# Optimization experiments

Measured on AMD Instinct MI355X. Metric: run time of the kernel, lower is better.

Reference implementation:

```python
import jax, jax.numpy as jnp
import numpy as np

B, N, E = 2, 16384, 262144          # batch, nodes, directed edges (avg deg 16)
K, D, Wm = 256, 3, 1                # nmodes, ndims, nmeasures
C, L, FC = 128, 4, 128              # channels, Fourier layers, fc hidden
IN_DIM, OUT_DIM = 3, 1


def setup_inputs() -> dict:
    key = jax.random.key(0)
    ks = jax.random.split(key, 20)
    s = 1.0 / (C * C)
    inp = {
        "x": jax.random.normal(ks[0], (B, N, IN_DIM), jnp.float32),
        "nodes": jax.random.uniform(ks[1], (B, N, D), jnp.float32),
        "node_mask": jnp.ones((B, N, 1), jnp.float32),
        "node_weights": jax.random.uniform(ks[2], (B, N, Wm), jnp.float32) / N,
        "directed_edges": jax.random.randint(ks[3], (B, E, 2), 0, N),
        "edge_gradient_weights": jax.random.normal(ks[4], (B, E, D), jnp.float32),
        "modes": jax.random.normal(ks[5], (K, D, Wm), jnp.float32),
        "sp_L": jnp.ones((D, Wm), jnp.float32),
        "weights_c": s * jax.random.uniform(ks[6], (L, C, C, K, Wm), jnp.float32),
        "weights_s": s * jax.random.uniform(ks[7], (L, C, C, K, Wm), jnp.float32),
        "weights_0": s * jax.random.uniform(ks[8], (L, C, C, 1, Wm), jnp.float32),
        "fc0_w": jax.random.normal(ks[9], (C, IN_DIM), jnp.float32) * 0.1,
        "fc0_b": jnp.zeros((C,), jnp.float32),
        "ws_w": jax.random.normal(ks[10], (L, C, C), jnp.float32) * 0.05,
        "ws_b": jnp.zeros((L, C), jnp.float32),
        "gws_w": jax.random.normal(ks[11], (L, C, D * C), jnp.float32) * 0.05,
        "gws_b": jnp.zeros((L, C), jnp.float32),
        "fc1_w": jax.random.normal(ks[12], (FC, C), jnp.float32) * 0.05,
        "fc1_b": jnp.zeros((FC,), jnp.float32),
        "fc2_w": jax.random.normal(ks[13], (OUT_DIM, FC), jnp.float32) * 0.05,
        "fc2_b": jnp.zeros((OUT_DIM,), jnp.float32),
    }
    return inp


def _gelu(x):
    return jax.nn.gelu(x, approximate=False)  # torch F.gelu default = exact erf


def _compute_gradient(f, directed_edges, edge_gradient_weights):
    # f: [B, C, N] -> gradients [B, C*D, N] via directed-edge scatter-add
    fT = jnp.transpose(f, (0, 2, 1))                       # [B, N, C]
    tgt, src = directed_edges[..., 0], directed_edges[..., 1]
    f_src = jnp.take_along_axis(fT, src[..., None], axis=1)  # [B, E, C]
    f_tgt = jnp.take_along_axis(fT, tgt[..., None], axis=1)
    msg = jnp.einsum('bed,bec->becd', edge_gradient_weights, f_src - f_tgt)
    msg = msg.reshape(msg.shape[0], msg.shape[1], -1)        # [B, E, C*D]

    def scat(m, t):
        return jnp.zeros((fT.shape[1], m.shape[-1]), m.dtype).at[t].add(m)

    g = jax.vmap(scat)(msg, tgt)                             # [B, N, C*D]
    return jnp.transpose(g, (0, 2, 1))


def _spectral_conv(x, wc, wsn, w0, bc, bs, b0, wbc, wbs, wb0):
    # x: [B, C_in, N]
    xc = jnp.einsum('bix,bxkw->bikw', x, wbc)
    xs = -jnp.einsum('bix,bxkw->bikw', x, wbs)
    x0 = jnp.einsum('bix,bxkw->bikw', x, wb0)
    fc = jnp.einsum('bikw,iokw->bokw', xc, wc) - jnp.einsum('bikw,iokw->bokw', xs, wsn)
    fs = jnp.einsum('bikw,iokw->bokw', xs, wc) + jnp.einsum('bikw,iokw->bokw', xc, wsn)
    f0 = jnp.einsum('bikw,iokw->bokw', x0, w0)
    return (jnp.einsum('bokw,bxkw->box', f0, b0)
            + 2.0 * jnp.einsum('bokw,bxkw->box', fc, bc)
            - 2.0 * jnp.einsum('bokw,bxkw->box', fs, bs))


def reference(x, nodes, node_mask, node_weights, directed_edges, edge_gradient_weights,
              modes, sp_L, weights_c, weights_s, weights_0,
              fc0_w, fc0_b, ws_w, ws_b, gws_w, gws_b, fc1_w, fc1_b, fc2_w, fc2_b):
    # Fourier bases with learnable length-scale sp_L: [K,D,Wm]*[D,Wm]
    temp = jnp.einsum('bxd,kdw->bxkw', nodes, modes * sp_L)   # [B,N,K,Wm]
    bc, bs = jnp.cos(temp), jnp.sin(temp)
    b0 = jnp.zeros((temp.shape[0], temp.shape[1], 1, temp.shape[3]), temp.dtype)
    nw = (node_weights * node_mask)[:, :, None, :]            # [B,N,1,Wm]
    wbc, wbs, wb0 = bc * nw, bs * nw, b0 * nw

    h = jnp.einsum('bxi,ci->bxc', x, fc0_w) + fc0_b           # lift [B,N,C]
    h = jnp.transpose(h, (0, 2, 1))                           # [B,C,N]

    for i in range(L):
        x1 = _spectral_conv(h, weights_c[i], weights_s[i], weights_0[i],
                            bc, bs, b0, wbc, wbs, wb0)
        x2 = jnp.einsum('oc,bcn->bon', ws_w[i], h) + ws_b[i][None, :, None]
        grad = _compute_gradient(h, directed_edges, edge_gradient_weights)
        x3 = jnp.einsum('og,bgn->bon', gws_w[i], grad) + gws_b[i][None, :, None]
        h = x1 + x2 + x3
        if i != L - 1:
            h = _gelu(h)

    h = jnp.transpose(h, (0, 2, 1))                           # [B,N,C]
    h = _gelu(jnp.einsum('bnc,fc->bnf', h, fc1_w) + fc1_b)
    out = jnp.einsum('bnf,of->bno', h, fc2_w) + fc2_b         # [B,N,out_dim]
    return out
```

## Files before the change

### kernel.cpp

```cpp
#include <hip/hip_runtime.h>
#include <math.h>

#define Bn 2
#define Nn 16384
#define En 262144
#define Kn 256
#define Cn 128
#define Rn 512
#define Ln 4
#define LDP 72
#define NSPLIT 64

typedef float f32x4 __attribute__((ext_vector_type(4)));
typedef short s16x8 __attribute__((ext_vector_type(8)));

__device__ __forceinline__ float gelu_f(float x){
  return 0.5f*x*(1.0f + erff(x*0.70710678118654752440f));
}
__device__ __forceinline__ unsigned short f2b(float x){
  unsigned int u = __float_as_uint(x);
  unsigned int r = (u + 0x7FFFu + ((u>>16)&1u)) >> 16;
  return (unsigned short)r;
}
__device__ __forceinline__ float b2f(unsigned short h){
  return __uint_as_float(((unsigned int)h)<<16);
}
__device__ __forceinline__ unsigned int pack2(float lo, float hi){
  return (unsigned int)f2b(lo) | ((unsigned int)f2b(hi) << 16);
}


__global__ __launch_bounds__(256) void k_nw(const float* __restrict__ nwt,
                                            const float* __restrict__ msk,
                                            float* __restrict__ nw){
  int i = blockIdx.x*256 + threadIdx.x;
  nw[i] = nwt[i]*msk[i];
}

__global__ __launch_bounds__(256) void k_basis(const float* __restrict__ nodes,
                                               const float* __restrict__ modes,
                                               const float* __restrict__ spl,
                                               unsigned short* __restrict__ basis,
                                               unsigned short* __restrict__ basisT){
  __shared__ unsigned short tile[32*520];
  int gn0 = blockIdx.x*32;
  int tid = threadIdx.x;
  float m0 = modes[tid*3+0]*spl[0];
  float m1 = modes[tid*3+1]*spl[1];
  float m2 = modes[tid*3+2]*spl[2];
  for (int j=0;j<32;j++){
    const float* nd = nodes + (size_t)(gn0+j)*3;
    float t = nd[0]*m0 + nd[1]*m1 + nd[2]*m2;
    float s,c;
    sincosf(t,&s,&c);
    tile[j*520 + tid]       = f2b(c);
    tile[j*520 + 256 + tid] = f2b(s);
  }
  __syncthreads();
  int row = tid>>3, col0 = (tid&7)*64;
  #pragma unroll
  for (int q=0;q<8;q++){
    s16x8 v = *(const s16x8*)&tile[row*520 + col0 + q*8];
    *(s16x8*)(basis + (size_t)(gn0+row)*Rn + col0 + q*8) = v;
  }
  int b = gn0 >> 14;
  int nl = gn0 & (Nn-1);
  #pragma unroll
  for (int h=0; h<2; h++){
    int r = h*256 + tid;
    unsigned short* dst = basisT + ((size_t)(b*Rn + r))*Nn + nl;
    #pragma unroll
    for (int q=0;q<4;q++){
      unsigned short tmp[8];
      #pragma unroll
      for (int e=0;e<8;e++) tmp[e] = tile[(q*8+e)*520 + r];
      *(s16x8*)(dst + q*8) = *(const s16x8*)tmp;
    }
  }
}

__global__ __launch_bounds__(256) void k_lift(const float* __restrict__ x,
                                              const float* __restrict__ w,
                                              const float* __restrict__ bias,
                                              const float* __restrict__ nw,
                                              unsigned short* __restrict__ hg,
                                              unsigned short* __restrict__ hpack,
                                              unsigned short* __restrict__ hwT){
  __shared__ float ht[64*132];
  int gn0 = blockIdx.x*64;
  int tid = threadIdx.x;
  int c = tid & 127, rh = tid >> 7;
  float w0 = w[c*3], w1 = w[c*3+1], w2 = w[c*3+2], bb = bias[c];
  for (int j=0;j<32;j++){
    int n = rh*32 + j;
    const float* xp = x + (size_t)(gn0+n)*3;
    float v = bb + xp[0]*w0 + xp[1]*w1 + xp[2]*w2;
    ht[n*132 + c] = v;
    unsigned short hv = f2b(v);
    hg[(size_t)(gn0+n)*Rn + c] = hv;
    hpack[(size_t)(gn0+n)*Cn + c] = hv;
  }
  __syncthreads();
  int b = gn0 >> 14, nl = gn0 & (Nn-1);
  int cc = tid>>1, hf = tid&1;
  unsigned short* dst = hwT + ((size_t)(b*Cn + cc))*Nn + nl + hf*32;
  #pragma unroll
  for (int q=0;q<8;q++){
    int n = hf*32 + q*4;
    float4 nv = *(const float4*)&nw[(size_t)b*Nn + nl + n];
    ushort4 pk;
    pk.x = f2b(ht[(n+0)*132+cc]*nv.x);
    pk.y = f2b(ht[(n+1)*132+cc]*nv.y);
    pk.z = f2b(ht[(n+2)*132+cc]*nv.z);
    pk.w = f2b(ht[(n+3)*132+cc]*nv.w);
    *(ushort4*)(dst + q*4) = pk;
  }
}

__global__ __launch_bounds__(128) void k_w2c(const float* __restrict__ ws_w,
                                             const float* __restrict__ ws_b,
                                             const float* __restrict__ gws_w,
                                             const float* __restrict__ gws_b,
                                             unsigned short* __restrict__ W2,
                                             float* __restrict__ bias2){
  int bid = blockIdx.x;
  int tid = threadIdx.x;
  unsigned short* wrow = W2 + (size_t)bid*Rn;
  wrow[tid] = f2b(ws_w[(size_t)bid*Cn + tid]);
  const float* g = gws_w + (size_t)bid*384;
  wrow[128+tid] = f2b(g[tid*3+0]);
  wrow[256+tid] = f2b(g[tid*3+1]);
  wrow[384+tid] = f2b(g[tid*3+2]);
  if (tid==0) bias2[bid] = ws_b[bid] + gws_b[bid];
}

__global__ __launch_bounds__(256) void k_cvt(const float* __restrict__ in,
                                             unsigned short* __restrict__ out, int n){
  int i = blockIdx.x*256 + threadIdx.x;
  if (i < n) out[i] = f2b(in[i]);
}


__global__ __launch_bounds__(256) void k_count(const int* __restrict__ de,
                                               int* __restrict__ cnt){
  int i = blockIdx.x*256 + threadIdx.x;
  int b = i >> 18;
  int tgt = de[(size_t)i*2];
  atomicAdd(&cnt[b*Nn + tgt], 1);
}

__global__ __launch_bounds__(1024) void k_scan(const int* __restrict__ cnt,
                                               int* __restrict__ rowptr,
                                               int* __restrict__ cursor){
  __shared__ int part[1024];
  int t = threadIdx.x;
  int b = t >> 9;
  int li = t & 511;
  int loc[32];
  int s = 0;
  int base = b*Nn + li*32;
  #pragma unroll
  for (int j=0;j<32;j++){ loc[j] = s; s += cnt[base+j]; }
  part[t] = s;
  __syncthreads();
  int run = s;
  for (int off=1; off<512; off<<=1){
    int v = (li >= off) ? part[t-off] : 0;
    __syncthreads();
    part[t] += v;
    __syncthreads();
  }
  int incl = part[t];
  int excl = incl - run;
  int rbase = b*(Nn+1) + li*32;
  #pragma unroll
  for (int j=0;j<32;j++){
    int val = excl + loc[j];
    rowptr[rbase+j] = val;
    cursor[base+j]  = val;
  }
  if (li == 511) rowptr[b*(Nn+1) + Nn] = incl;
}

__global__ __launch_bounds__(256) void k_fill(const int* __restrict__ de,
                                              const float* __restrict__ egw,
                                              int* __restrict__ cursor,
                                              float4* __restrict__ epack){
  int i = blockIdx.x*256 + threadIdx.x;
  int b = i >> 18;
  int tgt = de[(size_t)i*2];
  int src = de[(size_t)i*2+1];
  int pos = atomicAdd(&cursor[b*Nn + tgt], 1);
  const float* g = egw + (size_t)i*3;
  float4 pk;
  pk.x = __int_as_float(src);
  pk.y = g[0]; pk.z = g[1]; pk.w = g[2];
  epack[(size_t)b*En + pos] = pk;
}

__global__ __launch_bounds__(128) void k_grad(const unsigned short* __restrict__ hpack,
                                              const float4* __restrict__ epack,
                                              const int* __restrict__ rowptr,
                                              unsigned short* __restrict__ hg_w){
  int bid = blockIdx.x;
  int b = bid >> 14, n = bid & (Nn-1);
  int tid = threadIdx.x;
  int wv = tid >> 6;
  int l  = tid & 63;
  const unsigned short* hb = hpack + (size_t)b*Nn*Cn;
  unsigned int ft2 = *(const unsigned int*)(hb + (size_t)n*Cn + 2*l);
  float ftlo = b2f((unsigned short)(ft2 & 0xffffu));
  float fthi = b2f((unsigned short)(ft2 >> 16));
  int beg = rowptr[b*(Nn+1) + n];
  int end = rowptr[b*(Nn+1) + n + 1];
  const float4* ep = epack + (size_t)b*En;
  float a0lo=0.f,a0hi=0.f,a1lo=0.f,a1hi=0.f,a2lo=0.f,a2hi=0.f;
  int j = beg + wv;
  for (; j + 2 < end; j += 4){
    float4 pk0 = ep[j];
    float4 pk1 = ep[j+2];
    int s0 = __float_as_int(pk0.x);
    int s1 = __float_as_int(pk1.x);
    unsigned int h0 = *(const unsigned int*)(hb + (size_t)s0*Cn + 2*l);
    unsigned int h1 = *(const unsigned int*)(hb + (size_t)s1*Cn + 2*l);
    float d0lo = b2f((unsigned short)(h0 & 0xffffu)) - ftlo;
    float d0hi = b2f((unsigned short)(h0 >> 16))     - fthi;
    float d1lo = b2f((unsigned short)(h1 & 0xffffu)) - ftlo;
    float d1hi = b2f((unsigned short)(h1 >> 16))     - fthi;
    a0lo += pk0.y*d0lo + pk1.y*d1lo;  a0hi += pk0.y*d0hi + pk1.y*d1hi;
    a1lo += pk0.z*d0lo + pk1.z*d1lo;  a1hi += pk0.z*d0hi + pk1.z*d1hi;
    a2lo += pk0.w*d0lo + pk1.w*d1lo;  a2hi += pk0.w*d0hi + pk1.w*d1hi;
  }
  if (j < end){
    float4 pk = ep[j];
    int src = __float_as_int(pk.x);
    unsigned int hv = *(const unsigned int*)(hb + (size_t)src*Cn + 2*l);
    float dlo = b2f((unsigned short)(hv & 0xffffu)) - ftlo;
    float dhi = b2f((unsigned short)(hv >> 16))     - fthi;
    a0lo += pk.y*dlo; a0hi += pk.y*dhi;
    a1lo += pk.z*dlo; a1hi += pk.z*dhi;
    a2lo += pk.w*dlo; a2hi += pk.w*dhi;
  }
  __shared__ float red[64*7];
  if (wv == 1){
    float* r = &red[l*7];
    r[0]=a0lo; r[1]=a0hi; r[2]=a1lo; r[3]=a1hi; r[4]=a2lo; r[5]=a2hi;
  }
  __syncthreads();
  if (wv == 0){
    const float* r = &red[l*7];
    a0lo+=r[0]; a0hi+=r[1]; a1lo+=r[2]; a1hi+=r[3]; a2lo+=r[4]; a2hi+=r[5];
    unsigned short* o = hg_w + (size_t)bid*Rn + Cn;
    *(unsigned int*)(o + 2*l)       = pack2(a0lo, a0hi);
    *(unsigned int*)(o + 128 + 2*l) = pack2(a1lo, a1hi);
    *(unsigned int*)(o + 256 + 2*l) = pack2(a2lo, a2hi);
  }
}

__device__ __forceinline__ void stage_tile(const unsigned short* __restrict__ g, size_t ldg,
                                           unsigned short* __restrict__ lds, int tid){
  int row = tid >> 3;
  int seg = (tid & 7) * 8;
  #pragma unroll
  for (int rb=0; rb<4; rb++){
    s16x8 v = *(const s16x8*)(g + (size_t)(row + rb*32)*ldg + seg);
    *(s16x8*)(lds + (size_t)(row + rb*32)*LDP + seg) = v;
  }
}
__device__ __forceinline__ void stage_tile512(const unsigned short* __restrict__ g, size_t ldg,
                                              unsigned short* __restrict__ lds, int tid){
  int row = tid >> 3;
  int seg = (tid & 7) * 8;
  #pragma unroll
  for (int rb=0; rb<2; rb++){
    s16x8 v = *(const s16x8*)(g + (size_t)(row + rb*64)*ldg + seg);
    *(s16x8*)(lds + (size_t)(row + rb*64)*LDP + seg) = v;
  }
}

__device__ __forceinline__ void mfma_chunk(const unsigned short* __restrict__ As,
                                           const unsigned short* __restrict__ Bs,
                                           f32x4 acc[4][4], int wm, int wn, int lr, int lg){
  #pragma unroll
  for (int kk=0; kk<2; kk++){
    s16x8 a[4], b[4];
    #pragma unroll
    for (int i=0;i<4;i++)
      a[i] = *(const s16x8*)(As + (size_t)(wm*64 + i*16 + lr)*LDP + kk*32 + lg*8);
    #pragma unroll
    for (int i=0;i<4;i++)
      b[i] = *(const s16x8*)(Bs + (size_t)(wn*64 + i*16 + lr)*LDP + kk*32 + lg*8);
    #pragma unroll
    for (int i=0;i<4;i++)
      #pragma unroll
      for (int j=0;j<4;j++)
        acc[i][j] = __builtin_amdgcn_mfma_f32_16x16x32_bf16(a[i], b[j], acc[i][j], 0, 0, 0);
  }
}

__device__ __forceinline__ void mfma_chunk8(const unsigned short* __restrict__ As,
                                            const unsigned short* __restrict__ Bs,
                                            f32x4 acc[4][2], int wm, int wn, int lr, int lg){
  #pragma unroll
  for (int kk=0; kk<2; kk++){
    s16x8 a[4], b[2];
    #pragma unroll
    for (int i=0;i<4;i++)
      a[i] = *(const s16x8*)(As + (size_t)(wm*64 + i*16 + lr)*LDP + kk*32 + lg*8);
    #pragma unroll
    for (int j=0;j<2;j++)
      b[j] = *(const s16x8*)(Bs + (size_t)(wn*32 + j*16 + lr)*LDP + kk*32 + lg*8);
    #pragma unroll
    for (int i=0;i<4;i++)
      #pragma unroll
      for (int j=0;j<2;j++)
        acc[i][j] = __builtin_amdgcn_mfma_f32_16x16x32_bf16(a[i], b[j], acc[i][j], 0, 0, 0);
  }
}

__global__ __launch_bounds__(256) void k_fwd_mfma(const unsigned short* __restrict__ basisT,
                                                  const unsigned short* __restrict__ hwT,
                                                  float* __restrict__ part){
  __shared__ unsigned short As[128*LDP];
  __shared__ unsigned short Bs[128*LDP];
  int tid = threadIdx.x;
  int mt = blockIdx.x;
  int ks = blockIdx.y;
  int b  = blockIdx.z;
  const int KSP = Nn/NSPLIT;
  const unsigned short* A  = basisT + ((size_t)(b*Rn + mt*128))*Nn + (size_t)ks*KSP;
  const unsigned short* Bp = hwT   + ((size_t)(b*Cn))*Nn + (size_t)ks*KSP;
  f32x4 acc[4][4] = {};
  int l = tid & 63, w = tid >> 6, wm = w >> 1, wn = w & 1, lr = l & 15, lg = l >> 4;
  for (int k0 = 0; k0 < KSP; k0 += 64){
    stage_tile(A + k0, Nn, As, tid);
    stage_tile(Bp + k0, Nn, Bs, tid);
    __syncthreads();
    mfma_chunk(As, Bs, acc, wm, wn, lr, lg);
    __syncthreads();
  }
  float* pb = part + ((size_t)ks*Bn + b)*(Cn*Rn);
  int r0 = mt*128 + wm*64;
  int c0 = wn*64;
  #pragma unroll
  for (int i=0;i<4;i++)
    #pragma unroll
    for (int j=0;j<4;j++){
      int r = r0 + i*16 + lg*4;
      int c = c0 + j*16 + lr;
      *(f32x4*)&pb[(size_t)c*Rn + r] = acc[i][j];
    }
}

__global__ __launch_bounds__(256) void k_reduce(const float* __restrict__ part,
                                                float* __restrict__ xf){
  int idx = blockIdx.x*256 + threadIdx.x;
  float s = 0.f;
  #pragma unroll 8
  for (int ks=0; ks<NSPLIT; ks++)
    s += part[(size_t)ks*(Bn*Cn*Rn) + idx];
  xf[idx] = s;
}

__global__ __launch_bounds__(512) void k_mm(const float* __restrict__ xf,
                                            const float* __restrict__ wc,
                                            const float* __restrict__ ws,
                                            float* __restrict__ Fpart){
  int o  = blockIdx.x;
  int is = blockIdx.y;
  int tid = threadIdx.x;
  int half = tid >> 8, t = tid & 255;
  int ibase = is*64 + half*32;
  float fc0=0.f, fs0=0.f, fc1=0.f, fs1=0.f;
  for (int ii=0; ii<32; ii++){
    int i = ibase + ii;
    float wcv = wc[((size_t)i*Cn + o)*Kn + t];
    float wsv = ws[((size_t)i*Cn + o)*Kn + t];
    float x0c = xf[(size_t)i*Rn + t];
    float x0s = xf[(size_t)i*Rn + 256 + t];
    float x1c = xf[(size_t)Cn*Rn + (size_t)i*Rn + t];
    float x1s = xf[(size_t)Cn*Rn + (size_t)i*Rn + 256 + t];
    fc0 += x0c*wcv + x0s*wsv;  fs0 += x0c*wsv - x0s*wcv;
    fc1 += x1c*wcv + x1s*wsv;  fs1 += x1c*wsv - x1s*wcv;
  }
  __shared__ float red[4][256];
  if (half){ red[0][t]=fc0; red[1][t]=fs0; red[2][t]=fc1; red[3][t]=fs1; }
  __syncthreads();
  if (!half){
    fc0 += red[0][t]; fs0 += red[1][t];
    fc1 += red[2][t]; fs1 += red[3][t];
    float* f0 = Fpart + ((size_t)(is*Bn + 0)*Cn + o)*Rn;
    float* f1 = Fpart + ((size_t)(is*Bn + 1)*Cn + o)*Rn;
    f0[t]     = fc0;  f0[256+t] = fs0;
    f1[t]     = fc1;  f1[256+t] = fs1;
  }
}

__global__ __launch_bounds__(256) void k_fcvt(const float* __restrict__ Fpart,
                                              unsigned short* __restrict__ Fbf){
  int idx = blockIdx.x*256 + threadIdx.x;
  float s = Fpart[idx] + Fpart[idx + Bn*Cn*Rn];
  float sc = ((idx & 511) < 256) ? 2.f : -2.f;
  Fbf[idx] = f2b(sc*s);
}

template<int GELU, int WRITE_AUX>
__global__ __launch_bounds__(512) void k_invcomb(const unsigned short* __restrict__ basis,
                                                 const unsigned short* __restrict__ Fbf,
                                                 unsigned short* __restrict__ hg,
                                                 const unsigned short* __restrict__ W2l,
                                                 const float* __restrict__ bias2l,
                                                 const float* __restrict__ nw,
                                                 unsigned short* __restrict__ hpack,
                                                 unsigned short* __restrict__ hwT){
  __shared__ unsigned short As1[128*LDP];
  __shared__ unsigned short Bs1[128*LDP];
  __shared__ unsigned short As2[128*LDP];
  __shared__ unsigned short Bs2[128*LDP];
  int tid = threadIdx.x;
  int nt = blockIdx.x;
  int b  = blockIdx.y;
  size_t nbase = (size_t)b*Nn + (size_t)nt*128;
  f32x4 acc[4][2] = {};
  int l = tid & 63, w = tid >> 6, wm = w >> 2, wn = w & 3, lr = l & 15, lg = l >> 4;
  const unsigned short* A1 = basis + nbase*Rn;
  const unsigned short* B1 = Fbf + (size_t)b*Cn*Rn;
  const unsigned short* A2 = hg + nbase*Rn;
  for (int k0=0;k0<512;k0+=64){
    stage_tile512(A1+k0, Rn, As1, tid);
    stage_tile512(B1+k0, Rn, Bs1, tid);
    stage_tile512(A2+k0, Rn, As2, tid);
    stage_tile512(W2l+k0, Rn, Bs2, tid);
    __syncthreads();
    mfma_chunk8(As1,Bs1,acc,wm,wn,lr,lg);
    mfma_chunk8(As2,Bs2,acc,wm,wn,lr,lg);
    __syncthreads();
  }
  #pragma unroll
  for (int i=0;i<4;i++){
    int nloc = wm*64 + i*16 + lg*4;
    float4 w4;
    if (WRITE_AUX) w4 = *(const float4*)&nw[(size_t)b*Nn + nt*128 + nloc];
    #pragma unroll
    for (int j=0;j<2;j++){
      int c = wn*32 + j*16 + lr;
      float bsv = bias2l[c];
      float v[4];
      #pragma unroll
      for (int e=0;e<4;e++){
        v[e] = acc[i][j][e] + bsv;
        if (GELU) v[e] = gelu_f(v[e]);
        unsigned short hv = f2b(v[e]);
        hpack[(nbase + nloc + e)*Cn + c] = hv;
        if (WRITE_AUX) hg[(nbase + nloc + e)*Rn + c] = hv;
      }
      if (WRITE_AUX){
        ushort4 pk;
        pk.x = f2b(v[0]*w4.x); pk.y = f2b(v[1]*w4.y);
        pk.z = f2b(v[2]*w4.z); pk.w = f2b(v[3]*w4.w);
        *(ushort4*)&hwT[((size_t)(b*Cn + c))*Nn + nt*128 + nloc] = pk;
      }
    }
  }
}

__global__ __launch_bounds__(512) void k_fc1(const unsigned short* __restrict__ hpack,
                                             const unsigned short* __restrict__ fw,
                                             const float* __restrict__ fb,
                                             unsigned short* __restrict__ h2){
  __shared__ unsigned short As[128*LDP];
  __shared__ unsigned short Bs[128*LDP];
  int tid = threadIdx.x;
  int nt = blockIdx.x;
  int b  = blockIdx.y;
  size_t nbase = (size_t)b*Nn + (size_t)nt*128;
  f32x4 acc[4][2] = {};
  int l = tid & 63, w = tid >> 6, wm = w >> 2, wn = w & 3, lr = l & 15, lg = l >> 4;
  const unsigned short* A = hpack + nbase*Cn;
  for (int k0=0;k0<128;k0+=64){
    stage_tile512(A+k0, Cn, As, tid);
    stage_tile512(fw+k0, Cn, Bs, tid);
    __syncthreads();
    mfma_chunk8(As,Bs,acc,wm,wn,lr,lg);
    __syncthreads();
  }
  #pragma unroll
  for (int i=0;i<4;i++){
    int nloc = wm*64 + i*16 + lg*4;
    #pragma unroll
    for (int j=0;j<2;j++){
      int c = wn*32 + j*16 + lr;
      float bsv = fb[c];
      #pragma unroll
      for (int e=0;e<4;e++){
        float v = gelu_f(acc[i][j][e] + bsv);
        h2[(nbase + nloc + e)*Cn + c] = f2b(v);
      }
    }
  }
}

__global__ __launch_bounds__(256) void k_out(const unsigned short* __restrict__ h2,
                                             const float* __restrict__ w,
                                             const float* __restrict__ bptr,
                                             float* __restrict__ outp){
  int tid = threadIdx.x;
  int node = blockIdx.x*4 + (tid>>6);
  int f = tid & 63;
  const unsigned short* hp = h2 + (size_t)node*Cn;
  float s = b2f(hp[f])*w[f] + b2f(hp[f+64])*w[f+64];
  #pragma unroll
  for (int off=32; off>0; off>>=1) s += __shfl_down(s, off);
  if (f==0) outp[node] = s + bptr[0];
}

static constexpr size_t OB_BASIS  = 0;
static constexpr size_t OB_BASIST = OB_BASIS  + 33554432;
static constexpr size_t OB_HG     = OB_BASIST + 33554432;
static constexpr size_t OB_HWT    = OB_HG     + 33554432;
static constexpr size_t OB_H2     = OB_HWT    + 8388608;
static constexpr size_t OB_HP     = OB_H2     + 8388608;
static constexpr size_t OB_NW     = OB_HP     + 8388608;
static constexpr size_t OB_XF     = OB_NW     + 131072;
static constexpr size_t OB_FBF    = OB_XF     + 524288;
static constexpr size_t OB_FPART  = OB_FBF    + 262144;
static constexpr size_t OB_W2     = OB_FPART  + 1048576;
static constexpr size_t OB_B2     = OB_W2     + 524288;
static constexpr size_t OB_FC1W   = OB_B2     + 2048;
static constexpr size_t OB_EPACK  = OB_FC1W   + 32768;
static constexpr size_t OB_INT    = OB_EPACK  + 8388608;
static constexpr size_t OB_PART   = OB_INT    + 524288;

extern "C" void kernel_launch(void* const* d_in, const int* in_sizes, int n_in,
                              void* d_out, int out_size, void* d_ws, size_t ws_size,
                              hipStream_t stream) {
  const float* x            = (const float*)d_in[0];
  const float* nodes        = (const float*)d_in[1];
  const float* node_mask    = (const float*)d_in[2];
  const float* node_weights = (const float*)d_in[3];
  const int*   de           = (const int*)  d_in[4];
  const float* egw          = (const float*)d_in[5];
  const float* modes        = (const float*)d_in[6];
  const float* spl          = (const float*)d_in[7];
  const float* wc           = (const float*)d_in[8];
  const float* wsp          = (const float*)d_in[9];
  const float* fc0_w        = (const float*)d_in[11];
  const float* fc0_b        = (const float*)d_in[12];
  const float* ws_w         = (const float*)d_in[13];
  const float* ws_b         = (const float*)d_in[14];
  const float* gws_w        = (const float*)d_in[15];
  const float* gws_b        = (const float*)d_in[16];
  const float* fc1_w        = (const float*)d_in[17];
  const float* fc1_b        = (const float*)d_in[18];
  const float* fc2_w        = (const float*)d_in[19];
  const float* fc2_b        = (const float*)d_in[20];
  float* outp = (float*)d_out;

  char* wsb = (char*)d_ws;
  unsigned short* basis  = (unsigned short*)(wsb + OB_BASIS);
  unsigned short* basisT = (unsigned short*)(wsb + OB_BASIST);
  unsigned short* hg     = (unsigned short*)(wsb + OB_HG);
  unsigned short* hwT    = (unsigned short*)(wsb + OB_HWT);
  unsigned short* h2     = (unsigned short*)(wsb + OB_H2);
  unsigned short* hpack  = (unsigned short*)(wsb + OB_HP);
  float* nw              = (float*)(wsb + OB_NW);
  float* xf              = (float*)(wsb + OB_XF);
  unsigned short* Fbf    = (unsigned short*)(wsb + OB_FBF);
  float* Fpart           = (float*)(wsb + OB_FPART);
  unsigned short* W2     = (unsigned short*)(wsb + OB_W2);
  float* bias2           = (float*)(wsb + OB_B2);
  unsigned short* fc1wb  = (unsigned short*)(wsb + OB_FC1W);
  float4* epack          = (float4*)(wsb + OB_EPACK);
  int* count  = (int*)(wsb + OB_INT);
  int* rowptr = count + Bn*Nn;
  int* cursor = rowptr + Bn*(Nn+1);
  float* part = (float*)(wsb + OB_PART);

  k_nw<<<(Bn*Nn)/256, 256, 0, stream>>>(node_weights, node_mask, nw);
  k_basis<<<(Bn*Nn)/32, 256, 0, stream>>>(nodes, modes, spl, basis, basisT);
  k_lift<<<(Bn*Nn)/64, 256, 0, stream>>>(x, fc0_w, fc0_b, nw, hg, hpack, hwT);

  (void)hipMemsetAsync(count, 0, (size_t)Bn*Nn*sizeof(int), stream);
  k_count<<<(Bn*En)/256, 256, 0, stream>>>(de, count);
  k_scan<<<1, 1024, 0, stream>>>(count, rowptr, cursor);
  k_fill<<<(Bn*En)/256, 256, 0, stream>>>(de, egw, cursor, epack);

  k_w2c<<<Ln*Cn, 128, 0, stream>>>(ws_w, ws_b, gws_w, gws_b, W2, bias2);
  k_cvt<<<64, 256, 0, stream>>>(fc1_w, fc1wb, Cn*Cn);

  for (int l=0; l<Ln; l++){
    k_fwd_mfma<<<dim3(4,NSPLIT,2), 256, 0, stream>>>(basisT, hwT, part);
    k_reduce<<<(Bn*Cn*Rn)/256, 256, 0, stream>>>(part, xf);
    k_mm<<<dim3(Cn,2), 512, 0, stream>>>(xf, wc + (size_t)l*Cn*Cn*Kn,
                                         wsp + (size_t)l*Cn*Cn*Kn, Fpart);
    k_fcvt<<<(Bn*Cn*Rn)/256, 256, 0, stream>>>(Fpart, Fbf);
    k_grad<<<Bn*Nn, 128, 0, stream>>>(hpack, epack, rowptr, hg);
    if (l < Ln-1){
      k_invcomb<1,1><<<dim3(Nn/128,2), 512, 0, stream>>>(
          basis, Fbf, hg, W2 + (size_t)l*Cn*Rn, bias2 + l*Cn, nw, hpack, hwT);
    } else {
      k_invcomb<0,0><<<dim3(Nn/128,2), 512, 0, stream>>>(
          basis, Fbf, hg, W2 + (size_t)l*Cn*Rn, bias2 + l*Cn, nw, hpack, hwT);
    }
  }

  k_fc1<<<dim3(Nn/128,2), 512, 0, stream>>>(hpack, fc1wb, fc1_b, h2);
  k_out<<<(Bn*Nn)/4, 256, 0, stream>>>(h2, fc2_w, fc2_b, outp);
}
```

Measured before the change: 534.2 us.

## Merge forward spectral GEMM and gradient scatter into one launch, fuse F conversion

Combines the forward spectral transform GEMM and the edge-gradient kernel into a single heterogeneous launch, with the first block range doing MFMA tiles and the rest doing gradient gathers (two nodes per 256-thread block). This lets both kinds of work run concurrently and removes launches. It also folds the F partial-sum reduction and bf16 conversion into the inverse kernel's tile staging. The separate hg buffer is dropped: the inverse kernel now reads h from hpack and the gradients from a compact 384-wide buffer. The cost is that every inverse block repeats the F conversion and the fused kernel has mixed occupancy.

```diff
diff --git a/kernel.cpp b/kernel.cpp
--- a/kernel.cpp
+++ b/kernel.cpp
@@ -10,6 +10,7 @@
 #define Ln 4
 #define LDP 72
 #define NSPLIT 64
+#define FWDB (4*NSPLIT*Bn)
 
 typedef float f32x4 __attribute__((ext_vector_type(4)));
 typedef short s16x8 __attribute__((ext_vector_type(8)));
@@ -83,7 +84,6 @@
                                               const float* __restrict__ w,
                                               const float* __restrict__ bias,
                                               const float* __restrict__ nw,
-                                              unsigned short* __restrict__ hg,
                                               unsigned short* __restrict__ hpack,
                                               unsigned short* __restrict__ hwT){
   __shared__ float ht[64*132];
@@ -96,9 +96,7 @@
     const float* xp = x + (size_t)(gn0+n)*3;
     float v = bb + xp[0]*w0 + xp[1]*w1 + xp[2]*w2;
     ht[n*132 + c] = v;
-    unsigned short hv = f2b(v);
-    hg[(size_t)(gn0+n)*Rn + c] = hv;
-    hpack[(size_t)(gn0+n)*Cn + c] = hv;
+    hpack[(size_t)(gn0+n)*Cn + c] = f2b(v);
   }
   __syncthreads();
   int b = gn0 >> 14, nl = gn0 & (Nn-1);
@@ -198,15 +196,138 @@
   epack[(size_t)b*En + pos] = pk;
 }
 
-__global__ __launch_bounds__(128) void k_grad(const unsigned short* __restrict__ hpack,
-                                              const float4* __restrict__ epack,
-                                              const int* __restrict__ rowptr,
-                                              unsigned short* __restrict__ hg_w){
+__device__ __forceinline__ void stage_tile(const unsigned short* __restrict__ g, size_t ldg,
+                                           unsigned short* __restrict__ lds, int tid){
+  int row = tid >> 3;
+  int seg = (tid & 7) * 8;
+  #pragma unroll
+  for (int rb=0; rb<4; rb++){
+    s16x8 v = *(const s16x8*)(g + (size_t)(row + rb*32)*ldg + seg);
+    *(s16x8*)(lds + (size_t)(row + rb*32)*LDP + seg) = v;
+  }
+}
+__device__ __forceinline__ void stage_tile512(const unsigned short* __restrict__ g, size_t ldg,
+                                              unsigned short* __restrict__ lds, int tid){
+  int row = tid >> 3;
+  int seg = (tid & 7) * 8;
+  #pragma unroll
+  for (int rb=0; rb<2; rb++){
+    s16x8 v = *(const s16x8*)(g + (size_t)(row + rb*64)*ldg + seg);
+    *(s16x8*)(lds + (size_t)(row + rb*64)*LDP + seg) = v;
+  }
+}
+__device__ __forceinline__ void stage_F(const float* __restrict__ Fp, int b, int k0,
+                                        unsigned short* __restrict__ lds, int tid){
+  int row = tid >> 3;
+  int col0 = (tid & 7) * 8;
+  float sc = (k0 < 256) ? 2.f : -2.f;
+  #pragma unroll
+  for (int rb=0; rb<2; rb++){
+    int r = row + rb*64;
+    const float* p0 = Fp + ((size_t)b*Cn + r)*Rn + k0 + col0;
+    const float* p1 = p0 + (size_t)Bn*Cn*Rn;
+    f32x4 a0 = *(const f32x4*)p0;
+    f32x4 a1 = *(const f32x4*)(p0+4);
+    f32x4 c0 = *(const f32x4*)p1;
+    f32x4 c1 = *(const f32x4*)(p1+4);
+    unsigned short tmp[8];
+    #pragma unroll
+    for (int e=0;e<4;e++){
+      tmp[e]   = f2b((a0[e]+c0[e])*sc);
+      tmp[4+e] = f2b((a1[e]+c1[e])*sc);
+    }
+    *(s16x8*)(lds + (size_t)r*LDP + col0) = *(const s16x8*)tmp;
+  }
+}
+
+__device__ __forceinline__ void mfma_chunk(const unsigned short* __restrict__ As,
+                                           const unsigned short* __restrict__ Bs,
+                                           f32x4 acc[4][4], int wm, int wn, int lr, int lg){
+  #pragma unroll
+  for (int kk=0; kk<2; kk++){
+    s16x8 a[4], b[4];
+    #pragma unroll
+    for (int i=0;i<4;i++)
+      a[i] = *(const s16x8*)(As + (size_t)(wm*64 + i*16 + lr)*LDP + kk*32 + lg*8);
+    #pragma unroll
+    for (int i=0;i<4;i++)
+      b[i] = *(const s16x8*)(Bs + (size_t)(wn*64 + i*16 + lr)*LDP + kk*32 + lg*8);
+    #pragma unroll
+    for (int i=0;i<4;i++)
+      #pragma unroll
+      for (int j=0;j<4;j++)
+        acc[i][j] = __builtin_amdgcn_mfma_f32_16x16x32_bf16(a[i], b[j], acc[i][j], 0, 0, 0);
+  }
+}
+
+__device__ __forceinline__ void mfma_chunk8(const unsigned short* __restrict__ As,
+                                            const unsigned short* __restrict__ Bs,
+                                            f32x4 acc[4][2], int wm, int wn, int lr, int lg){
+  #pragma unroll
+  for (int kk=0; kk<2; kk++){
+    s16x8 a[4], b[2];
+    #pragma unroll
+    for (int i=0;i<4;i++)
+      a[i] = *(const s16x8*)(As + (size_t)(wm*64 + i*16 + lr)*LDP + kk*32 + lg*8);
+    #pragma unroll
+    for (int j=0;j<2;j++)
+      b[j] = *(const s16x8*)(Bs + (size_t)(wn*32 + j*16 + lr)*LDP + kk*32 + lg*8);
+    #pragma unroll
+    for (int i=0;i<4;i++)
+      #pragma unroll
+      for (int j=0;j<2;j++)
+        acc[i][j] = __builtin_amdgcn_mfma_f32_16x16x32_bf16(a[i], b[j], acc[i][j], 0, 0, 0);
+  }
+}
+
+__global__ __launch_bounds__(256) void k_fg(const unsigned short* __restrict__ basisT,
+                                            const unsigned short* __restrict__ hwT,
+                                            float* __restrict__ part,
+                                            const unsigned short* __restrict__ hpack,
+                                            const float4* __restrict__ epack,
+                                            const int* __restrict__ rowptr,
+                                            unsigned short* __restrict__ gradbuf){
+  __shared__ unsigned char smem[2*128*LDP*2];
   int bid = blockIdx.x;
-  int b = bid >> 14, n = bid & (Nn-1);
-  int tid = threadIdx.x;
-  int wv = tid >> 6;
+  int tid = threadIdx.x;
+  if (bid < FWDB){
+    unsigned short* As = (unsigned short*)smem;
+    unsigned short* Bs = As + 128*LDP;
+    int mt = bid & 3;
+    int ks = (bid >> 2) & (NSPLIT-1);
+    int b  = bid >> 8;
+    const int KSP = Nn/NSPLIT;
+    const unsigned short* A  = basisT + ((size_t)(b*Rn + mt*128))*Nn + (size_t)ks*KSP;
+    const unsigned short* Bp = hwT   + ((size_t)(b*Cn))*Nn + (size_t)ks*KSP;
+    f32x4 acc[4][4] = {};
+    int l = tid & 63, w = tid >> 6, wm = w >> 1, wn = w & 1, lr = l & 15, lg = l >> 4;
+    for (int k0 = 0; k0 < KSP; k0 += 64){
+      stage_tile(A + k0, Nn, As, tid);
+      stage_tile(Bp + k0, Nn, Bs, tid);
+      __syncthreads();
+      mfma_chunk(As, Bs, acc, wm, wn, lr, lg);
+      __syncthreads();
+    }
+    float* pb = part + ((size_t)ks*Bn + b)*(Cn*Rn);
+    int r0 = mt*128 + wm*64;
+    int c0 = wn*64;
+    #pragma unroll
+    for (int i=0;i<4;i++)
+      #pragma unroll
+      for (int j=0;j<4;j++){
+        int r = r0 + i*16 + lg*4;
+        int c = c0 + j*16 + lr;
+        *(f32x4*)&pb[(size_t)c*Rn + r] = acc[i][j];
+      }
+    return;
+  }
+  float* red = (float*)smem;
+  int g = bid - FWDB;
+  int b = g >> 13;
+  int n = ((g & 8191) << 1) | (tid >> 7);
+  int wv = (tid >> 6) & 1;
   int l  = tid & 63;
+  int half = tid >> 7;
   const unsigned short* hb = hpack + (size_t)b*Nn*Cn;
   unsigned int ft2 = *(const unsigned int*)(hb + (size_t)n*Cn + 2*l);
   float ftlo = b2f((unsigned short)(ft2 & 0xffffu));
@@ -241,115 +362,19 @@
     a1lo += pk.z*dlo; a1hi += pk.z*dhi;
     a2lo += pk.w*dlo; a2hi += pk.w*dhi;
   }
-  __shared__ float red[64*7];
   if (wv == 1){
-    float* r = &red[l*7];
+    float* r = &red[(half*64 + l)*7];
     r[0]=a0lo; r[1]=a0hi; r[2]=a1lo; r[3]=a1hi; r[4]=a2lo; r[5]=a2hi;
   }
   __syncthreads();
   if (wv == 0){
-    const float* r = &red[l*7];
+    const float* r = &red[(half*64 + l)*7];
     a0lo+=r[0]; a0hi+=r[1]; a1lo+=r[2]; a1hi+=r[3]; a2lo+=r[4]; a2hi+=r[5];
-    unsigned short* o = hg_w + (size_t)bid*Rn + Cn;
+    unsigned short* o = gradbuf + ((size_t)b*Nn + n)*384;
     *(unsigned int*)(o + 2*l)       = pack2(a0lo, a0hi);
     *(unsigned int*)(o + 128 + 2*l) = pack2(a1lo, a1hi);
     *(unsigned int*)(o + 256 + 2*l) = pack2(a2lo, a2hi);
   }
-}
-
-__device__ __forceinline__ void stage_tile(const unsigned short* __restrict__ g, size_t ldg,
-                                           unsigned short* __restrict__ lds, int tid){
-  int row = tid >> 3;
-  int seg = (tid & 7) * 8;
-  #pragma unroll
-  for (int rb=0; rb<4; rb++){
-    s16x8 v = *(const s16x8*)(g + (size_t)(row + rb*32)*ldg + seg);
-    *(s16x8*)(lds + (size_t)(row + rb*32)*LDP + seg) = v;
-  }
-}
-__device__ __forceinline__ void stage_tile512(const unsigned short* __restrict__ g, size_t ldg,
-                                              unsigned short* __restrict__ lds, int tid){
-  int row = tid >> 3;
-  int seg = (tid & 7) * 8;
-  #pragma unroll
-  for (int rb=0; rb<2; rb++){
-    s16x8 v = *(const s16x8*)(g + (size_t)(row + rb*64)*ldg + seg);
-    *(s16x8*)(lds + (size_t)(row + rb*64)*LDP + seg) = v;
-  }
-}
-
-__device__ __forceinline__ void mfma_chunk(const unsigned short* __restrict__ As,
-                                           const unsigned short* __restrict__ Bs,
-                                           f32x4 acc[4][4], int wm, int wn, int lr, int lg){
-  #pragma unroll
-  for (int kk=0; kk<2; kk++){
-    s16x8 a[4], b[4];
-    #pragma unroll
-    for (int i=0;i<4;i++)
-      a[i] = *(const s16x8*)(As + (size_t)(wm*64 + i*16 + lr)*LDP + kk*32 + lg*8);
-    #pragma unroll
-    for (int i=0;i<4;i++)
-      b[i] = *(const s16x8*)(Bs + (size_t)(wn*64 + i*16 + lr)*LDP + kk*32 + lg*8);
-    #pragma unroll
-    for (int i=0;i<4;i++)
-      #pragma unroll
-      for (int j=0;j<4;j++)
-        acc[i][j] = __builtin_amdgcn_mfma_f32_16x16x32_bf16(a[i], b[j], acc[i][j], 0, 0, 0);
-  }
-}
-
-__device__ __forceinline__ void mfma_chunk8(const unsigned short* __restrict__ As,
-                                            const unsigned short* __restrict__ Bs,
-                                            f32x4 acc[4][2], int wm, int wn, int lr, int lg){
-  #pragma unroll
-  for (int kk=0; kk<2; kk++){
-    s16x8 a[4], b[2];
-    #pragma unroll
-    for (int i=0;i<4;i++)
-      a[i] = *(const s16x8*)(As + (size_t)(wm*64 + i*16 + lr)*LDP + kk*32 + lg*8);
-    #pragma unroll
-    for (int j=0;j<2;j++)
-      b[j] = *(const s16x8*)(Bs + (size_t)(wn*32 + j*16 + lr)*LDP + kk*32 + lg*8);
-    #pragma unroll
-    for (int i=0;i<4;i++)
-      #pragma unroll
-      for (int j=0;j<2;j++)
-        acc[i][j] = __builtin_amdgcn_mfma_f32_16x16x32_bf16(a[i], b[j], acc[i][j], 0, 0, 0);
-  }
-}
-
-__global__ __launch_bounds__(256) void k_fwd_mfma(const unsigned short* __restrict__ basisT,
-                                                  const unsigned short* __restrict__ hwT,
-                                                  float* __restrict__ part){
-  __shared__ unsigned short As[128*LDP];
-  __shared__ unsigned short Bs[128*LDP];
-  int tid = threadIdx.x;
-  int mt = blockIdx.x;
-  int ks = blockIdx.y;
-  int b  = blockIdx.z;
-  const int KSP = Nn/NSPLIT;
-  const unsigned short* A  = basisT + ((size_t)(b*Rn + mt*128))*Nn + (size_t)ks*KSP;
-  const unsigned short* Bp = hwT   + ((size_t)(b*Cn))*Nn + (size_t)ks*KSP;
-  f32x4 acc[4][4] = {};
-  int l = tid & 63, w = tid >> 6, wm = w >> 1, wn = w & 1, lr = l & 15, lg = l >> 4;
-  for (int k0 = 0; k0 < KSP; k0 += 64){
-    stage_tile(A + k0, Nn, As, tid);
-    stage_tile(Bp + k0, Nn, Bs, tid);
-    __syncthreads();
-    mfma_chunk(As, Bs, acc, wm, wn, lr, lg);
-    __syncthreads();
-  }
-  float* pb = part + ((size_t)ks*Bn + b)*(Cn*Rn);
-  int r0 = mt*128 + wm*64;
-  int c0 = wn*64;
-  #pragma unroll
-  for (int i=0;i<4;i++)
-    #pragma unroll
-    for (int j=0;j<4;j++){
-      int r = r0 + i*16 + lg*4;
-      int c = c0 + j*16 + lr;
-      *(f32x4*)&pb[(size_t)c*Rn + r] = acc[i][j];
-    }
 }
 
 __global__ __launch_bounds__(256) void k_reduce(const float* __restrict__ part,
@@ -396,18 +421,10 @@
   }
 }
 
-__global__ __launch_bounds__(256) void k_fcvt(const float* __restrict__ Fpart,
-                                              unsigned short* __restrict__ Fbf){
-  int idx = blockIdx.x*256 + threadIdx.x;
-  float s = Fpart[idx] + Fpart[idx + Bn*Cn*Rn];
-  float sc = ((idx & 511) < 256) ? 2.f : -2.f;
-  Fbf[idx] = f2b(sc*s);
-}
-
 template<int GELU, int WRITE_AUX>
 __global__ __launch_bounds__(512) void k_invcomb(const unsigned short* __restrict__ basis,
-                                                 const unsigned short* __restrict__ Fbf,
-                                                 unsigned short* __restrict__ hg,
+                                                 const float* __restrict__ Fpart,
+                                                 const unsigned short* __restrict__ gradbuf,
                                                  const unsigned short* __restrict__ W2l,
                                                  const float* __restrict__ bias2l,
                                                  const float* __restrict__ nw,
@@ -424,12 +441,11 @@
   f32x4 acc[4][2] = {};
   int l = tid & 63, w = tid >> 6, wm = w >> 2, wn = w & 3, lr = l & 15, lg = l >> 4;
   const unsigned short* A1 = basis + nbase*Rn;
-  const unsigned short* B1 = Fbf + (size_t)b*Cn*Rn;
-  const unsigned short* A2 = hg + nbase*Rn;
   for (int k0=0;k0<512;k0+=64){
     stage_tile512(A1+k0, Rn, As1, tid);
-    stage_tile512(B1+k0, Rn, Bs1, tid);
-    stage_tile512(A2+k0, Rn, As2, tid);
+    stage_F(Fpart, b, k0, Bs1, tid);
+    if (k0 < 128) stage_tile512(hpack + nbase*Cn + k0, Cn, As2, tid);
+    else          stage_tile512(gradbuf + nbase*384 + (k0-128), 384, As2, tid);
     stage_tile512(W2l+k0, Rn, Bs2, tid);
     __syncthreads();
     mfma_chunk8(As1,Bs1,acc,wm,wn,lr,lg);
@@ -450,9 +466,7 @@
       for (int e=0;e<4;e++){
         v[e] = acc[i][j][e] + bsv;
         if (GELU) v[e] = gelu_f(v[e]);
-        unsigned short hv = f2b(v[e]);
-        hpack[(nbase + nloc + e)*Cn + c] = hv;
-        if (WRITE_AUX) hg[(nbase + nloc + e)*Rn + c] = hv;
+        hpack[(nbase + nloc + e)*Cn + c] = f2b(v[e]);
       }
       if (WRITE_AUX){
         ushort4 pk;
@@ -516,14 +530,13 @@
 
 static constexpr size_t OB_BASIS  = 0;
 static constexpr size_t OB_BASIST = OB_BASIS  + 33554432;
-static constexpr size_t OB_HG     = OB_BASIST + 33554432;
-static constexpr size_t OB_HWT    = OB_HG     + 33554432;
+static constexpr size_t OB_GRAD   = OB_BASIST + 33554432;
+static constexpr size_t OB_HWT    = OB_GRAD   + 25165824;
 static constexpr size_t OB_H2     = OB_HWT    + 8388608;
 static constexpr size_t OB_HP     = OB_H2     + 8388608;
 static constexpr size_t OB_NW     = OB_HP     + 8388608;
 static constexpr size_t OB_XF     = OB_NW     + 131072;
-static constexpr size_t OB_FBF    = OB_XF     + 524288;
-static constexpr size_t OB_FPART  = OB_FBF    + 262144;
+static constexpr size_t OB_FPART  = OB_XF     + 524288;
 static constexpr size_t OB_W2     = OB_FPART  + 1048576;
 static constexpr size_t OB_B2     = OB_W2     + 524288;
 static constexpr size_t OB_FC1W   = OB_B2     + 2048;
@@ -557,20 +570,19 @@
   float* outp = (float*)d_out;
 
   char* wsb = (char*)d_ws;
-  unsigned short* basis  = (unsigned short*)(wsb + OB_BASIS);
-  unsigned short* basisT = (unsigned short*)(wsb + OB_BASIST);
-  unsigned short* hg     = (unsigned short*)(wsb + OB_HG);
-  unsigned short* hwT    = (unsigned short*)(wsb + OB_HWT);
-  unsigned short* h2     = (unsigned short*)(wsb + OB_H2);
-  unsigned short* hpack  = (unsigned short*)(wsb + OB_HP);
-  float* nw              = (float*)(wsb + OB_NW);
-  float* xf              = (float*)(wsb + OB_XF);
-  unsigned short* Fbf    = (unsigned short*)(wsb + OB_FBF);
-  float* Fpart           = (float*)(wsb + OB_FPART);
-  unsigned short* W2     = (unsigned short*)(wsb + OB_W2);
-  float* bias2           = (float*)(wsb + OB_B2);
-  unsigned short* fc1wb  = (unsigned short*)(wsb + OB_FC1W);
-  float4* epack          = (float4*)(wsb + OB_EPACK);
+  unsigned short* basis   = (unsigned short*)(wsb + OB_BASIS);
+  unsigned short* basisT  = (unsigned short*)(wsb + OB_BASIST);
+  unsigned short* gradbuf = (unsigned short*)(wsb + OB_GRAD);
+  unsigned short* hwT     = (unsigned short*)(wsb + OB_HWT);
+  unsigned short* h2      = (unsigned short*)(wsb + OB_H2);
+  unsigned short* hpack   = (unsigned short*)(wsb + OB_HP);
+  float* nw               = (float*)(wsb + OB_NW);
+  float* xf               = (float*)(wsb + OB_XF);
+  float* Fpart            = (float*)(wsb + OB_FPART);
+  unsigned short* W2      = (unsigned short*)(wsb + OB_W2);
+  float* bias2            = (float*)(wsb + OB_B2);
+  unsigned short* fc1wb   = (unsigned short*)(wsb + OB_FC1W);
+  float4* epack           = (float4*)(wsb + OB_EPACK);
   int* count  = (int*)(wsb + OB_INT);
   int* rowptr = count + Bn*Nn;
   int* cursor = rowptr + Bn*(Nn+1);
@@ -578,7 +590,7 @@
 
   k_nw<<<(Bn*Nn)/256, 256, 0, stream>>>(node_weights, node_mask, nw);
   k_basis<<<(Bn*Nn)/32, 256, 0, stream>>>(nodes, modes, spl, basis, basisT);
-  k_lift<<<(Bn*Nn)/64, 256, 0, stream>>>(x, fc0_w, fc0_b, nw, hg, hpack, hwT);
+  k_lift<<<(Bn*Nn)/64, 256, 0, stream>>>(x, fc0_w, fc0_b, nw, hpack, hwT);
 
   (void)hipMemsetAsync(count, 0, (size_t)Bn*Nn*sizeof(int), stream);
   k_count<<<(Bn*En)/256, 256, 0, stream>>>(de, count);
@@ -589,18 +601,17 @@
   k_cvt<<<64, 256, 0, stream>>>(fc1_w, fc1wb, Cn*Cn);
 
   for (int l=0; l<Ln; l++){
-    k_fwd_mfma<<<dim3(4,NSPLIT,2), 256, 0, stream>>>(basisT, hwT, part);
+    k_fg<<<FWDB + (Bn*Nn)/2, 256, 0, stream>>>(basisT, hwT, part,
+                                               hpack, epack, rowptr, gradbuf);
     k_reduce<<<(Bn*Cn*Rn)/256, 256, 0, stream>>>(part, xf);
     k_mm<<<dim3(Cn,2), 512, 0, stream>>>(xf, wc + (size_t)l*Cn*Cn*Kn,
                                          wsp + (size_t)l*Cn*Cn*Kn, Fpart);
-    k_fcvt<<<(Bn*Cn*Rn)/256, 256, 0, stream>>>(Fpart, Fbf);
-    k_grad<<<Bn*Nn, 128, 0, stream>>>(hpack, epack, rowptr, hg);
     if (l < Ln-1){
       k_invcomb<1,1><<<dim3(Nn/128,2), 512, 0, stream>>>(
-          basis, Fbf, hg, W2 + (size_t)l*Cn*Rn, bias2 + l*Cn, nw, hpack, hwT);
+          basis, Fpart, gradbuf, W2 + (size_t)l*Cn*Rn, bias2 + l*Cn, nw, hpack, hwT);
     } else {
       k_invcomb<0,0><<<dim3(Nn/128,2), 512, 0, stream>>>(
-          basis, Fbf, hg, W2 + (size_t)l*Cn*Rn, bias2 + l*Cn, nw, hpack, hwT);
+          basis, Fpart, gradbuf, W2 + (size_t)l*Cn*Rn, bias2 + l*Cn, nw, hpack, hwT);
     }
   }
 
```

Result: slower. 637.2 us (+19.3%).
